# Optimization experiments

Hardware: AMD Instinct MI355X
Metric: run time of the kernel (lower is better)

The kernel has to match this reference:

```python
import jax, jax.numpy as jnp
import numpy as np

N_NODES = 100000
N_EDGES = 1600000
HIDDEN = 64


def setup_inputs() -> dict:
    key = jax.random.key(0)
    ks = jax.random.split(key, 10)
    s = 0.1
    x = jax.random.normal(ks[0], (N_NODES, 1), dtype=jnp.float32)
    edge_index = jax.random.randint(ks[1], (2, N_EDGES), 0, N_NODES, dtype=jnp.int32)
    edge_weight = jnp.ones((N_EDGES,), dtype=jnp.float32)
    f32 = jnp.float32
    return {
        "x": x,
        "edge_weight": edge_weight,
        "Wz": jax.random.normal(ks[2], (1, HIDDEN), f32) * s,
        "bz": jnp.zeros((HIDDEN,), f32),
        "Lz": jax.random.normal(ks[3], (2 * HIDDEN, HIDDEN), f32) * s,
        "lbz": jnp.zeros((HIDDEN,), f32),
        "Wr": jax.random.normal(ks[4], (1, HIDDEN), f32) * s,
        "br": jnp.zeros((HIDDEN,), f32),
        "Lr": jax.random.normal(ks[5], (2 * HIDDEN, HIDDEN), f32) * s,
        "lbr": jnp.zeros((HIDDEN,), f32),
        "Wh": jax.random.normal(ks[6], (1, HIDDEN), f32) * s,
        "bh": jnp.zeros((HIDDEN,), f32),
        "Lh": jax.random.normal(ks[7], (2 * HIDDEN, HIDDEN), f32) * s,
        "lbh": jnp.zeros((HIDDEN,), f32),
        "Wout": jax.random.normal(ks[8], (HIDDEN, 1), f32) * s,
        "bout": jnp.zeros((1,), f32),
        "edge_index": edge_index,
    }


def reference(x, edge_weight, Wz, bz, Lz, lbz, Wr, br, Lr, lbr,
              Wh, bh, Lh, lbh, Wout, bout, edge_index):
    N = x.shape[0]
    hidden = Wz.shape[1]
    src, dst = edge_index[0], edge_index[1]
    # GCN normalization with added self-loops (PyG gcn_norm)
    loop = jnp.arange(N, dtype=src.dtype)
    src2 = jnp.concatenate([src, loop])
    dst2 = jnp.concatenate([dst, loop])
    ew2 = jnp.concatenate([edge_weight, jnp.ones((N,), x.dtype)])
    deg = jax.ops.segment_sum(ew2, dst2, num_segments=N)  # [N]
    dinv = jnp.where(deg > 0, jax.lax.rsqrt(deg), 0.0)
    norm = dinv[src2] * ew2 * dinv[dst2]  # [E+N]

    def gcn(W, b):
        xw = x @ W  # [N, H]
        agg = jax.ops.segment_sum(xw[src2] * norm[:, None], dst2, num_segments=N)
        return agg + b

    # TGCN cell with H0 = 0 (no hidden state passed)
    H = jnp.zeros((N, hidden), x.dtype)
    Z = jax.nn.sigmoid(jnp.concatenate([gcn(Wz, bz), H], axis=1) @ Lz + lbz)
    R = jax.nn.sigmoid(jnp.concatenate([gcn(Wr, br), H], axis=1) @ Lr + lbr)
    Ht = jnp.tanh(jnp.concatenate([gcn(Wh, bh), H * R], axis=1) @ Lh + lbh)
    Hn = Z * H + (1.0 - Z) * Ht
    h = jax.nn.relu(Hn)
    return h @ Wout + bout
```

## Files before the change

kernel.cpp:

```cpp
#include <hip/hip_runtime.h>
#include <math.h>

#define HIDDEN 64
#define RANGE 16384
#define RSHIFT 14
#define G 32
#define NB 256
#define MAXR 8
#define PACK_SHIFT 17

__global__ __launch_bounds__(256)
void k_compact(const int* __restrict__ dst, const int* __restrict__ src,
               const float* __restrict__ ew, uint2* __restrict__ comp,
               int* __restrict__ gcur, int E, int capE) {
    __shared__ int hist[MAXR];
    __shared__ int rbase[MAXR];
    __shared__ int cur[MAXR];
    if (threadIdx.x < MAXR) hist[threadIdx.x] = 0;
    __syncthreads();

    long long e0 = (((long long)E * blockIdx.x) / NB) & ~3LL;
    long long e1 = (blockIdx.x == NB - 1) ? (long long)E
                                          : ((((long long)E * (blockIdx.x + 1)) / NB) & ~3LL);
    const int nvec = (int)((e1 - e0) >> 2);
    const int4*   dst4 = (const int4*)(dst + e0);
    const int4*   src4 = (const int4*)(src + e0);
    const float4* ew4  = (const float4*)(ew + e0);

    for (int i = threadIdx.x; i < nvec; i += blockDim.x) {
        int4 d = dst4[i];
        atomicAdd(&hist[d.x >> RSHIFT], 1);
        atomicAdd(&hist[d.y >> RSHIFT], 1);
        atomicAdd(&hist[d.z >> RSHIFT], 1);
        atomicAdd(&hist[d.w >> RSHIFT], 1);
    }
    for (long long e = e0 + ((long long)nvec << 2) + threadIdx.x; e < e1; e += blockDim.x)
        atomicAdd(&hist[dst[e] >> RSHIFT], 1);
    __syncthreads();

    if (threadIdx.x < MAXR) {
        rbase[threadIdx.x] = atomicAdd(&gcur[threadIdx.x], hist[threadIdx.x]);
        cur[threadIdx.x] = 0;
    }
    __syncthreads();

    for (int i = threadIdx.x; i < nvec; i += blockDim.x) {
        int4   d = dst4[i];
        int4   s = src4[i];
        float4 t = ew4[i];
        int   dd[4] = {d.x, d.y, d.z, d.w};
        int   ss[4] = {s.x, s.y, s.z, s.w};
        float tt[4] = {t.x, t.y, t.z, t.w};
        #pragma unroll
        for (int j = 0; j < 4; ++j) {
            int r = dd[j] >> RSHIFT;
            int pos = atomicAdd(&cur[r], 1);
            comp[(size_t)r * capE + rbase[r] + pos] =
                make_uint2(((unsigned)(dd[j] & (RANGE - 1)) << PACK_SHIFT) | (unsigned)ss[j],
                           __float_as_uint(tt[j]));
        }
    }
    for (long long e = e0 + ((long long)nvec << 2) + threadIdx.x; e < e1; e += blockDim.x) {
        int d = dst[e];
        int r = d >> RSHIFT;
        int pos = atomicAdd(&cur[r], 1);
        comp[(size_t)r * capE + rbase[r] + pos] =
            make_uint2(((unsigned)(d & (RANGE - 1)) << PACK_SHIFT) | (unsigned)src[e],
                       __float_as_uint(ew[e]));
    }
}

template <bool WEIGHTED>
__global__ __launch_bounds__(1024)
void k_bin(const uint2* __restrict__ comp, const int* __restrict__ gcur,
           const float* __restrict__ w, float* __restrict__ partials,
           int nranges, int capE) {
    __shared__ float bins[RANGE];
    float4* b4 = (float4*)bins;
    for (int i = threadIdx.x; i < RANGE / 4; i += blockDim.x)
        b4[i] = make_float4(0.f, 0.f, 0.f, 0.f);
    __syncthreads();

    const int r = blockIdx.x / G, c = blockIdx.x % G;
    const int len = gcur[r];
    const uint2* bucket = comp + (size_t)r * capE;
    const int a0 = (int)((long long)len * c / G);
    const int a1 = (int)((long long)len * (c + 1) / G);

    for (int i = a0 + threadIdx.x; i < a1; i += blockDim.x) {
        uint2 e = bucket[i];
        float v = __uint_as_float(e.y);
        if (WEIGHTED) v *= w[e.x & ((1u << PACK_SHIFT) - 1u)];
        atomicAdd(&bins[e.x >> PACK_SHIFT], v);
    }
    __syncthreads();

    float4* outp = (float4*)(partials + ((size_t)c * nranges + r) * RANGE);
    for (int i = threadIdx.x; i < RANGE / 4; i += blockDim.x) outp[i] = b4[i];
}

__global__ void k_node(const float* __restrict__ x, const float* __restrict__ partials,
                       float* __restrict__ dinv, float* __restrict__ w,
                       int N, int nranges,
                       const float* __restrict__ Wz, const float* __restrict__ bz,
                       const float* __restrict__ Lz, const float* __restrict__ lbz,
                       const float* __restrict__ Wh, const float* __restrict__ bh,
                       const float* __restrict__ Lh, const float* __restrict__ lbh,
                       float* __restrict__ coeff) {
    int i = blockIdx.x * blockDim.x + threadIdx.x;
    if (i < N) {
        int r = i >> RSHIFT, local = i & (RANGE - 1);
        const float* p = partials + (size_t)r * RANGE + local;
        float d = 1.0f;
        #pragma unroll
        for (int c = 0; c < G; ++c) d += p[(size_t)c * nranges * RANGE];
        float di = rsqrtf(d);
        dinv[i] = di;
        w[i] = di * x[i];
    }
    if (blockIdx.x == 0 && threadIdx.x < HIDDEN) {
        int j = threadIdx.x;
        float vz = 0.f, cz = 0.f, vh = 0.f, ch = 0.f;
        for (int k = 0; k < HIDDEN; ++k) {
            float lz = Lz[k * HIDDEN + j];
            float lh = Lh[k * HIDDEN + j];
            vz += Wz[k] * lz;
            cz += bz[k] * lz;
            vh += Wh[k] * lh;
            ch += bh[k] * lh;
        }
        coeff[j]       = vz;
        coeff[64 + j]  = cz + lbz[j];
        coeff[128 + j] = vh;
        coeff[192 + j] = ch + lbh[j];
    }
}

__global__ void k_out(const float* __restrict__ partials, const float* __restrict__ dinv,
                      const float* __restrict__ w, const float* __restrict__ coeff,
                      const float* __restrict__ Wout, const float* __restrict__ bout,
                      float* __restrict__ out, int N, int nranges) {
    __shared__ float c[5 * HIDDEN];
    __shared__ float b0;
    if (threadIdx.x < 4 * HIDDEN) c[threadIdx.x] = coeff[threadIdx.x];
    if (threadIdx.x < HIDDEN) c[4 * HIDDEN + threadIdx.x] = Wout[threadIdx.x];
    if (threadIdx.x == 0) b0 = bout[0];
    __syncthreads();
    int i = blockIdx.x * blockDim.x + threadIdx.x;
    if (i < N) {
        int r = i >> RSHIFT, local = i & (RANGE - 1);
        const float* p = partials + (size_t)r * RANGE + local;
        float g = w[i];
        #pragma unroll
        for (int k = 0; k < G; ++k) g += p[(size_t)k * nranges * RANGE];
        float si = dinv[i] * g;
        float acc = b0;
        #pragma unroll
        for (int j = 0; j < HIDDEN; ++j) {
            float zp = fminf(fmaxf(si * c[j] + c[64 + j], -30.f), 30.f);
            float hp = fminf(fmaxf(si * c[128 + j] + c[192 + j], -15.f), 15.f);
            float a  = __expf(2.0f * hp);
            float t  = (a - 1.0f) / (a + 1.0f);
            float zn = 1.0f / (1.0f + __expf(zp));
            float hn = zn * t;
            hn = hn > 0.0f ? hn : 0.0f;
            acc = fmaf(hn, c[256 + j], acc);
        }
        out[i] = acc;
    }
}

extern "C" void kernel_launch(void* const* d_in, const int* in_sizes, int n_in,
                              void* d_out, int out_size, void* d_ws, size_t ws_size,
                              hipStream_t stream) {
    const float* x    = (const float*)d_in[0];
    const float* ew   = (const float*)d_in[1];
    const float* Wz   = (const float*)d_in[2];
    const float* bz   = (const float*)d_in[3];
    const float* Lz   = (const float*)d_in[4];
    const float* lbz  = (const float*)d_in[5];
    const float* Wh   = (const float*)d_in[10];
    const float* bh   = (const float*)d_in[11];
    const float* Lh   = (const float*)d_in[12];
    const float* lbh  = (const float*)d_in[13];
    const float* Wout = (const float*)d_in[14];
    const float* bout = (const float*)d_in[15];
    const int*   eidx = (const int*)d_in[16];

    const int N = in_sizes[0];
    const int E = in_sizes[1];
    const int* src = eidx;
    const int* dst = eidx + E;

    const int nranges = (N + RANGE - 1) / RANGE;
    const int capE = E;

    float* partials = (float*)d_ws;
    uint2* comp     = (uint2*)(partials + (size_t)G * nranges * RANGE);
    float* dinv     = (float*)(comp + (size_t)nranges * capE);
    float* w        = dinv + N;
    float* coeff    = w + N;
    int*   gcur     = (int*)(coeff + 4 * HIDDEN);

    const int TB = 256;
    const int grid_bin = nranges * G;

    hipMemsetAsync(gcur, 0, MAXR * sizeof(int), stream);
    k_compact<<<NB, 256, 0, stream>>>(dst, src, ew, comp, gcur, E, capE);
    k_bin<false><<<grid_bin, 1024, 0, stream>>>(comp, gcur, (const float*)nullptr,
                                                partials, nranges, capE);
    k_node<<<(N + TB - 1) / TB, TB, 0, stream>>>(x, partials, dinv, w, N, nranges,
                                                 Wz, bz, Lz, lbz, Wh, bh, Lh, lbh, coeff);
    k_bin<true><<<grid_bin, 1024, 0, stream>>>(comp, gcur, w, partials, nranges, capE);
    k_out<<<(N + TB - 1) / TB, TB, 0, stream>>>(partials, dinv, w, coeff, Wout, bout,
                                                (float*)d_out, N, nranges);
}
```

Baseline: 158.1 us.

## Fuse degree normalization into binning via last-block reduction, halve bin chunk count

The separate per-node degree kernel is removed. Each range's last-finishing degree-bin block, detected with an atomic counter, now reduces the partials and writes dinv and w. The coefficient precompute moves into the compaction kernel. G is halved from 32 to 16, so there are fewer partial histograms to write and reduce, at the cost of less parallelism in the binning kernels. This saves a launch but serializes the final reduction onto one block per range.

After: 225.1 us. 42.4% more time.

```diff
diff --git a/kernel.cpp b/kernel.cpp
--- a/kernel.cpp
+++ b/kernel.cpp
@@ -4,7 +4,7 @@
 #define HIDDEN 64
 #define RANGE 16384
 #define RSHIFT 14
-#define G 32
+#define G 16
 #define NB 256
 #define MAXR 8
 #define PACK_SHIFT 17
@@ -12,112 +12,16 @@
 __global__ __launch_bounds__(256)
 void k_compact(const int* __restrict__ dst, const int* __restrict__ src,
                const float* __restrict__ ew, uint2* __restrict__ comp,
-               int* __restrict__ gcur, int E, int capE) {
+               int* __restrict__ gcur, int E, int capE,
+               const float* __restrict__ Wz, const float* __restrict__ bz,
+               const float* __restrict__ Lz, const float* __restrict__ lbz,
+               const float* __restrict__ Wh, const float* __restrict__ bh,
+               const float* __restrict__ Lh, const float* __restrict__ lbh,
+               float* __restrict__ coeff) {
     __shared__ int hist[MAXR];
     __shared__ int rbase[MAXR];
     __shared__ int cur[MAXR];
-    if (threadIdx.x < MAXR) hist[threadIdx.x] = 0;
-    __syncthreads();
-
-    long long e0 = (((long long)E * blockIdx.x) / NB) & ~3LL;
-    long long e1 = (blockIdx.x == NB - 1) ? (long long)E
-                                          : ((((long long)E * (blockIdx.x + 1)) / NB) & ~3LL);
-    const int nvec = (int)((e1 - e0) >> 2);
-    const int4*   dst4 = (const int4*)(dst + e0);
-    const int4*   src4 = (const int4*)(src + e0);
-    const float4* ew4  = (const float4*)(ew + e0);
-
-    for (int i = threadIdx.x; i < nvec; i += blockDim.x) {
-        int4 d = dst4[i];
-        atomicAdd(&hist[d.x >> RSHIFT], 1);
-        atomicAdd(&hist[d.y >> RSHIFT], 1);
-        atomicAdd(&hist[d.z >> RSHIFT], 1);
-        atomicAdd(&hist[d.w >> RSHIFT], 1);
-    }
-    for (long long e = e0 + ((long long)nvec << 2) + threadIdx.x; e < e1; e += blockDim.x)
-        atomicAdd(&hist[dst[e] >> RSHIFT], 1);
-    __syncthreads();
-
-    if (threadIdx.x < MAXR) {
-        rbase[threadIdx.x] = atomicAdd(&gcur[threadIdx.x], hist[threadIdx.x]);
-        cur[threadIdx.x] = 0;
-    }
-    __syncthreads();
-
-    for (int i = threadIdx.x; i < nvec; i += blockDim.x) {
-        int4   d = dst4[i];
-        int4   s = src4[i];
-        float4 t = ew4[i];
-        int   dd[4] = {d.x, d.y, d.z, d.w};
-        int   ss[4] = {s.x, s.y, s.z, s.w};
-        float tt[4] = {t.x, t.y, t.z, t.w};
-        #pragma unroll
-        for (int j = 0; j < 4; ++j) {
-            int r = dd[j] >> RSHIFT;
-            int pos = atomicAdd(&cur[r], 1);
-            comp[(size_t)r * capE + rbase[r] + pos] =
-                make_uint2(((unsigned)(dd[j] & (RANGE - 1)) << PACK_SHIFT) | (unsigned)ss[j],
-                           __float_as_uint(tt[j]));
-        }
-    }
-    for (long long e = e0 + ((long long)nvec << 2) + threadIdx.x; e < e1; e += blockDim.x) {
-        int d = dst[e];
-        int r = d >> RSHIFT;
-        int pos = atomicAdd(&cur[r], 1);
-        comp[(size_t)r * capE + rbase[r] + pos] =
-            make_uint2(((unsigned)(d & (RANGE - 1)) << PACK_SHIFT) | (unsigned)src[e],
-                       __float_as_uint(ew[e]));
-    }
-}
-
-template <bool WEIGHTED>
-__global__ __launch_bounds__(1024)
-void k_bin(const uint2* __restrict__ comp, const int* __restrict__ gcur,
-           const float* __restrict__ w, float* __restrict__ partials,
-           int nranges, int capE) {
-    __shared__ float bins[RANGE];
-    float4* b4 = (float4*)bins;
-    for (int i = threadIdx.x; i < RANGE / 4; i += blockDim.x)
-        b4[i] = make_float4(0.f, 0.f, 0.f, 0.f);
-    __syncthreads();
-
-    const int r = blockIdx.x / G, c = blockIdx.x % G;
-    const int len = gcur[r];
-    const uint2* bucket = comp + (size_t)r * capE;
-    const int a0 = (int)((long long)len * c / G);
-    const int a1 = (int)((long long)len * (c + 1) / G);
-
-    for (int i = a0 + threadIdx.x; i < a1; i += blockDim.x) {
-        uint2 e = bucket[i];
-        float v = __uint_as_float(e.y);
-        if (WEIGHTED) v *= w[e.x & ((1u << PACK_SHIFT) - 1u)];
-        atomicAdd(&bins[e.x >> PACK_SHIFT], v);
-    }
-    __syncthreads();
-
-    float4* outp = (float4*)(partials + ((size_t)c * nranges + r) * RANGE);
-    for (int i = threadIdx.x; i < RANGE / 4; i += blockDim.x) outp[i] = b4[i];
-}
-
-__global__ void k_node(const float* __restrict__ x, const float* __restrict__ partials,
-                       float* __restrict__ dinv, float* __restrict__ w,
-                       int N, int nranges,
-                       const float* __restrict__ Wz, const float* __restrict__ bz,
-                       const float* __restrict__ Lz, const float* __restrict__ lbz,
-                       const float* __restrict__ Wh, const float* __restrict__ bh,
-                       const float* __restrict__ Lh, const float* __restrict__ lbh,
-                       float* __restrict__ coeff) {
-    int i = blockIdx.x * blockDim.x + threadIdx.x;
-    if (i < N) {
-        int r = i >> RSHIFT, local = i & (RANGE - 1);
-        const float* p = partials + (size_t)r * RANGE + local;
-        float d = 1.0f;
-        #pragma unroll
-        for (int c = 0; c < G; ++c) d += p[(size_t)c * nranges * RANGE];
-        float di = rsqrtf(d);
-        dinv[i] = di;
-        w[i] = di * x[i];
-    }
+
     if (blockIdx.x == 0 && threadIdx.x < HIDDEN) {
         int j = threadIdx.x;
         float vz = 0.f, cz = 0.f, vh = 0.f, ch = 0.f;
@@ -134,6 +38,136 @@
         coeff[128 + j] = vh;
         coeff[192 + j] = ch + lbh[j];
     }
+
+    if (threadIdx.x < MAXR) hist[threadIdx.x] = 0;
+    __syncthreads();
+
+    long long e0 = (((long long)E * blockIdx.x) / NB) & ~3LL;
+    long long e1 = (blockIdx.x == NB - 1) ? (long long)E
+                                          : ((((long long)E * (blockIdx.x + 1)) / NB) & ~3LL);
+    const int nvec = (int)((e1 - e0) >> 2);
+    const int4*   dst4 = (const int4*)(dst + e0);
+    const int4*   src4 = (const int4*)(src + e0);
+    const float4* ew4  = (const float4*)(ew + e0);
+
+    for (int i = threadIdx.x; i < nvec; i += blockDim.x) {
+        int4 d = dst4[i];
+        atomicAdd(&hist[d.x >> RSHIFT], 1);
+        atomicAdd(&hist[d.y >> RSHIFT], 1);
+        atomicAdd(&hist[d.z >> RSHIFT], 1);
+        atomicAdd(&hist[d.w >> RSHIFT], 1);
+    }
+    for (long long e = e0 + ((long long)nvec << 2) + threadIdx.x; e < e1; e += blockDim.x)
+        atomicAdd(&hist[dst[e] >> RSHIFT], 1);
+    __syncthreads();
+
+    if (threadIdx.x < MAXR) {
+        rbase[threadIdx.x] = atomicAdd(&gcur[threadIdx.x], hist[threadIdx.x]);
+        cur[threadIdx.x] = 0;
+    }
+    __syncthreads();
+
+    for (int i = threadIdx.x; i < nvec; i += blockDim.x) {
+        int4   d = dst4[i];
+        int4   s = src4[i];
+        float4 t = ew4[i];
+        int   dd[4] = {d.x, d.y, d.z, d.w};
+        int   ss[4] = {s.x, s.y, s.z, s.w};
+        float tt[4] = {t.x, t.y, t.z, t.w};
+        #pragma unroll
+        for (int j = 0; j < 4; ++j) {
+            int r = dd[j] >> RSHIFT;
+            int pos = atomicAdd(&cur[r], 1);
+            comp[(size_t)r * capE + rbase[r] + pos] =
+                make_uint2(((unsigned)(dd[j] & (RANGE - 1)) << PACK_SHIFT) | (unsigned)ss[j],
+                           __float_as_uint(tt[j]));
+        }
+    }
+    for (long long e = e0 + ((long long)nvec << 2) + threadIdx.x; e < e1; e += blockDim.x) {
+        int d = dst[e];
+        int r = d >> RSHIFT;
+        int pos = atomicAdd(&cur[r], 1);
+        comp[(size_t)r * capE + rbase[r] + pos] =
+            make_uint2(((unsigned)(d & (RANGE - 1)) << PACK_SHIFT) | (unsigned)src[e],
+                       __float_as_uint(ew[e]));
+    }
+}
+
+__global__ __launch_bounds__(1024)
+void k_degnode(const uint2* __restrict__ comp, const int* __restrict__ gcur,
+               const float* __restrict__ x, float* __restrict__ partials,
+               float* __restrict__ dinv, float* __restrict__ w,
+               int* __restrict__ cnt, int N, int nranges, int capE) {
+    __shared__ float bins[RANGE];
+    __shared__ int is_last;
+    float4* b4 = (float4*)bins;
+    for (int i = threadIdx.x; i < RANGE / 4; i += blockDim.x)
+        b4[i] = make_float4(0.f, 0.f, 0.f, 0.f);
+    __syncthreads();
+
+    const int r = blockIdx.x / G, c = blockIdx.x % G;
+    const int len = gcur[r];
+    const uint2* bucket = comp + (size_t)r * capE;
+    const int a0 = (int)((long long)len * c / G);
+    const int a1 = (int)((long long)len * (c + 1) / G);
+
+    for (int i = a0 + threadIdx.x; i < a1; i += blockDim.x) {
+        uint2 e = bucket[i];
+        atomicAdd(&bins[e.x >> PACK_SHIFT], __uint_as_float(e.y));
+    }
+    __syncthreads();
+
+    float4* outp = (float4*)(partials + ((size_t)c * nranges + r) * RANGE);
+    for (int i = threadIdx.x; i < RANGE / 4; i += blockDim.x) outp[i] = b4[i];
+
+    __threadfence();
+    if (threadIdx.x == 0) {
+        int t = __hip_atomic_fetch_add(&cnt[r], 1, __ATOMIC_ACQ_REL,
+                                       __HIP_MEMORY_SCOPE_AGENT);
+        is_last = (t == G - 1);
+    }
+    __syncthreads();
+    if (!is_last) return;
+    __threadfence();
+
+    const int base = r * RANGE;
+    const int rsize = min(RANGE, N - base);
+    for (int i = threadIdx.x; i < rsize; i += blockDim.x) {
+        float d = 1.0f;
+        #pragma unroll
+        for (int k = 0; k < G; ++k)
+            d += partials[((size_t)k * nranges + r) * RANGE + i];
+        float di = rsqrtf(d);
+        dinv[base + i] = di;
+        w[base + i] = di * x[base + i];
+    }
+}
+
+__global__ __launch_bounds__(1024)
+void k_aggbin(const uint2* __restrict__ comp, const int* __restrict__ gcur,
+              const float* __restrict__ w, float* __restrict__ partials,
+              int nranges, int capE) {
+    __shared__ float bins[RANGE];
+    float4* b4 = (float4*)bins;
+    for (int i = threadIdx.x; i < RANGE / 4; i += blockDim.x)
+        b4[i] = make_float4(0.f, 0.f, 0.f, 0.f);
+    __syncthreads();
+
+    const int r = blockIdx.x / G, c = blockIdx.x % G;
+    const int len = gcur[r];
+    const uint2* bucket = comp + (size_t)r * capE;
+    const int a0 = (int)((long long)len * c / G);
+    const int a1 = (int)((long long)len * (c + 1) / G);
+
+    for (int i = a0 + threadIdx.x; i < a1; i += blockDim.x) {
+        uint2 e = bucket[i];
+        float v = w[e.x & ((1u << PACK_SHIFT) - 1u)] * __uint_as_float(e.y);
+        atomicAdd(&bins[e.x >> PACK_SHIFT], v);
+    }
+    __syncthreads();
+
+    float4* outp = (float4*)(partials + ((size_t)c * nranges + r) * RANGE);
+    for (int i = threadIdx.x; i < RANGE / 4; i += blockDim.x) outp[i] = b4[i];
 }
 
 __global__ void k_out(const float* __restrict__ partials, const float* __restrict__ dinv,
@@ -201,17 +235,17 @@
     float* w        = dinv + N;
     float* coeff    = w + N;
     int*   gcur     = (int*)(coeff + 4 * HIDDEN);
+    int*   cnt      = gcur + MAXR;
 
     const int TB = 256;
     const int grid_bin = nranges * G;
 
-    hipMemsetAsync(gcur, 0, MAXR * sizeof(int), stream);
-    k_compact<<<NB, 256, 0, stream>>>(dst, src, ew, comp, gcur, E, capE);
-    k_bin<false><<<grid_bin, 1024, 0, stream>>>(comp, gcur, (const float*)nullptr,
-                                                partials, nranges, capE);
-    k_node<<<(N + TB - 1) / TB, TB, 0, stream>>>(x, partials, dinv, w, N, nranges,
-                                                 Wz, bz, Lz, lbz, Wh, bh, Lh, lbh, coeff);
-    k_bin<true><<<grid_bin, 1024, 0, stream>>>(comp, gcur, w, partials, nranges, capE);
+    hipMemsetAsync(gcur, 0, 2 * MAXR * sizeof(int), stream);
+    k_compact<<<NB, 256, 0, stream>>>(dst, src, ew, comp, gcur, E, capE,
+                                      Wz, bz, Lz, lbz, Wh, bh, Lh, lbh, coeff);
+    k_degnode<<<grid_bin, 1024, 0, stream>>>(comp, gcur, x, partials, dinv, w,
+                                             cnt, N, nranges, capE);
+    k_aggbin<<<grid_bin, 1024, 0, stream>>>(comp, gcur, w, partials, nranges, capE);
     k_out<<<(N + TB - 1) / TB, TB, 0, stream>>>(partials, dinv, w, coeff, Wout, bout,
                                                 (float*)d_out, N, nranges);
 }
```
